# Kernel tuning notes

Hardware: AMD Instinct MI355X
Metric: run time of the kernel (lower is better)

Reference implementation:

```python
import jax, jax.numpy as jnp
import numpy as np

N_NODES = 100000


def sage_conv(x, src, dst, W_l, W_r, b):
    """PyG SAGEConv with mean aggregation: lin_l(mean_{j in N(i)} x_j) + lin_r(x_i) + b."""
    n = x.shape[0]
    msg = jax.ops.segment_sum(x[src], dst, num_segments=n)          # [N, C] sum of neighbor feats
    deg = jax.ops.segment_sum(jnp.ones_like(src, dtype=x.dtype), dst, num_segments=n)  # [N]
    agg = msg / jnp.maximum(deg, 1.0)[:, None]                      # mean aggregate
    return agg @ W_l + x @ W_r + b


def setup_inputs() -> dict:
    key = jax.random.key(0)
    ks = jax.random.split(key, 10)
    in_ch, hid, out_ch = 128, 128, 1
    E = 640000
    scale_in = 1.0 / np.sqrt(in_ch)
    scale_h = 1.0 / np.sqrt(hid)
    return {
        "x": jax.random.normal(ks[0], (N_NODES, in_ch), dtype=jnp.float32),
        "edge_index": jax.random.randint(ks[1], (2, E), 0, N_NODES, dtype=jnp.int64),
        "W1l": jax.random.normal(ks[2], (in_ch, hid), dtype=jnp.float32) * scale_in,
        "W1r": jax.random.normal(ks[3], (in_ch, hid), dtype=jnp.float32) * scale_in,
        "b1": jnp.zeros((hid,), dtype=jnp.float32),
        "W2l": jax.random.normal(ks[4], (hid, hid), dtype=jnp.float32) * scale_h,
        "W2r": jax.random.normal(ks[5], (hid, hid), dtype=jnp.float32) * scale_h,
        "b2": jnp.zeros((hid,), dtype=jnp.float32),
        "Wfc": jax.random.normal(ks[6], (hid, out_ch), dtype=jnp.float32) * scale_h,
        "bfc": jnp.zeros((out_ch,), dtype=jnp.float32),
    }


def reference(x, edge_index, W1l, W1r, b1, W2l, W2r, b2, Wfc, bfc):
    src, dst = edge_index[0], edge_index[1]
    h = sage_conv(x, src, dst, W1l, W1r, b1)
    h = jax.nn.relu(h)
    # dropout p=0.2 is identity in eval mode (training=False)
    h = sage_conv(h, src, dst, W2l, W2r, b2)
    h = jax.nn.relu(h)
    return jax.nn.sigmoid(h @ Wfc + bfc)
```

## Files before the change

### kernel.cpp

```cpp
#include <hip/hip_runtime.h>
#include <cstdint>

#define NN 100000
#define CH 128
#define NT_BLK 32
#define SCAN_B 256

typedef __bf16 bf16x8 __attribute__((ext_vector_type(8)));
typedef __bf16 bf16x4 __attribute__((ext_vector_type(4)));
typedef float  f32x4  __attribute__((ext_vector_type(4)));

__device__ __forceinline__ float b2f(unsigned short u) {
    union { unsigned int i; float f; } v; v.i = ((unsigned int)u) << 16; return v.f;
}

__global__ __launch_bounds__(256) void k_init(
    const float* __restrict__ x, unsigned short* __restrict__ xb,
    const float* __restrict__ W1l, const float* __restrict__ W1r,
    const float* __restrict__ W2l, const float* __restrict__ W2r,
    __bf16* __restrict__ wB, int* __restrict__ cnt)
{
    const int gtid = blockIdx.x * 256 + threadIdx.x;
    const int gsz = gridDim.x * 256;
    for (int i = gtid; i < NN; i += gsz) cnt[i] = 0;
    for (int i = gtid; i < NN * CH / 8; i += gsz) {
        const float4 a = *reinterpret_cast<const float4*>(x + (size_t)i * 8);
        const float4 c = *reinterpret_cast<const float4*>(x + (size_t)i * 8 + 4);
        bf16x8 o;
        o[0] = (__bf16)a.x; o[1] = (__bf16)a.y; o[2] = (__bf16)a.z; o[3] = (__bf16)a.w;
        o[4] = (__bf16)c.x; o[5] = (__bf16)c.y; o[6] = (__bf16)c.z; o[7] = (__bf16)c.w;
        *reinterpret_cast<bf16x8*>(xb + (size_t)i * 8) = o;
    }
    if (gtid < 8192) {
        const int l    = gtid >> 12;
        const int rem  = gtid & 4095;
        const int kt   = rem >> 9;
        const int nt   = (rem >> 6) & 7;
        const int lane = rem & 63;
        const float* Wl = l ? W2l : W1l;
        const float* Wr = l ? W2r : W1r;
        const int nn = nt * 16 + (lane & 15);
        const int k0 = kt * 32 + (lane >> 4) * 8;
        bf16x8 v;
#pragma unroll
        for (int i = 0; i < 8; ++i) {
            const int k = k0 + i;
            const float f = (k < CH) ? Wl[k * CH + nn] : Wr[(k - CH) * CH + nn];
            v[i] = (__bf16)f;
        }
        *reinterpret_cast<bf16x8*>(wB + (size_t)gtid * 8) = v;
    }
}

__global__ void k_count(const int* __restrict__ dst, int* __restrict__ cnt,
                        int* __restrict__ slot, int E) {
    const int e = blockIdx.x * blockDim.x + threadIdx.x;
    if (e < E) slot[e] = atomicAdd(&cnt[dst[e]], 1);
}

__global__ void k_scan(const int* __restrict__ cnt, int* __restrict__ rowptr,
                       int* __restrict__ bsum, int n) {
    __shared__ int tmp[SCAN_B];
    const int t = threadIdx.x;
    const int i = blockIdx.x * SCAN_B + t;
    const int v = (i < n) ? cnt[i] : 0;
    tmp[t] = v;
    __syncthreads();
    for (int off = 1; off < SCAN_B; off <<= 1) {
        const int tv = (t >= off) ? tmp[t - off] : 0;
        __syncthreads();
        tmp[t] += tv;
        __syncthreads();
    }
    if (i < n) rowptr[i] = tmp[t] - v;
    if (t == SCAN_B - 1) bsum[blockIdx.x] = tmp[SCAN_B - 1];
}

__global__ void k_add(int* __restrict__ rowptr, const int* __restrict__ bsum, int n, int E) {
    __shared__ int sd[SCAN_B];
    const int t = threadIdx.x;
    int s = 0;
    for (int j = t; j < (int)blockIdx.x; j += SCAN_B) s += bsum[j];
    sd[t] = s;
    __syncthreads();
    for (int off = SCAN_B / 2; off > 0; off >>= 1) {
        if (t < off) sd[t] += sd[t + off];
        __syncthreads();
    }
    const int base = sd[0];
    const int i = blockIdx.x * SCAN_B + t;
    if (i < n) rowptr[i] += base;
    if (i == 0) rowptr[n] = E;
}

__global__ void k_fill(const int* __restrict__ src, const int* __restrict__ dst,
                       const int* __restrict__ slot, const int* __restrict__ rowptr,
                       int* __restrict__ csr, int E) {
    const int e = blockIdx.x * blockDim.x + threadIdx.x;
    if (e < E) csr[rowptr[dst[e]] + slot[e]] = src[e];
}

template<bool FC>
__global__ __launch_bounds__(256) void k_layer(
    const unsigned short* __restrict__ feat,
    const int* __restrict__ rowptr, const int* __restrict__ csr,
    const bf16x8* __restrict__ wfrag,
    const float* __restrict__ bias,
    const float* __restrict__ Wfc, const float* __restrict__ bfc,
    void* __restrict__ outv)
{
    __shared__ unsigned short a_lds[NT_BLK * 256];
    __shared__ float red[4][16];
    char* lb = (char*)a_lds;
    const int tid = threadIdx.x;
    const int node0 = blockIdx.x * NT_BLK;

    const int g = tid >> 5;
    const int q = tid & 31;

#pragma unroll
    for (int it = 0; it < NT_BLK / 8; ++it) {
        const int r = it * 8 + g;
        const int node = node0 + r;
        const int swz = (r & 7) << 4;
        float4 s = make_float4(0.f, 0.f, 0.f, 0.f);
        bf16x4 k2 = {(__bf16)0.f, (__bf16)0.f, (__bf16)0.f, (__bf16)0.f};
        if (node < NN) {
            const int r0 = rowptr[node], r1 = rowptr[node + 1];
            const int last = r1 - 1;
            for (int rr = r0; rr < r1; rr += 8) {
                ushort4 uv[8];
                float mk[8];
#pragma unroll
                for (int u = 0; u < 8; ++u) {
                    const int p = rr + u;
                    const int idx = csr[p <= last ? p : last];
                    uv[u] = *reinterpret_cast<const ushort4*>(feat + (size_t)idx * CH + q * 4);
                    mk[u] = (p < r1) ? 1.f : 0.f;
                }
#pragma unroll
                for (int u = 0; u < 8; ++u) {
                    s.x += mk[u] * b2f(uv[u].x);
                    s.y += mk[u] * b2f(uv[u].y);
                    s.z += mk[u] * b2f(uv[u].z);
                    s.w += mk[u] * b2f(uv[u].w);
                }
            }
            const float invd = 1.0f / fmaxf((float)(r1 - r0), 1.0f);
            s.x *= invd; s.y *= invd; s.z *= invd; s.w *= invd;
            const ushort4 u = *reinterpret_cast<const ushort4*>(feat + (size_t)node * CH + q * 4);
            k2 = *reinterpret_cast<const bf16x4*>(&u);
        }
        bf16x4 a;
        a[0] = (__bf16)s.x; a[1] = (__bf16)s.y; a[2] = (__bf16)s.z; a[3] = (__bf16)s.w;
        *reinterpret_cast<bf16x4*>(lb + r * 512 + ((q * 8) ^ swz)) = a;
        *reinterpret_cast<bf16x4*>(lb + r * 512 + ((256 + q * 8) ^ swz)) = k2;
    }
    __syncthreads();

    const int lane = tid & 63;
    const int w = tid >> 6;
    const int rows16 = (w >> 1) * 16;
    const int ntbase = (w & 1) * 4;
    const int row = rows16 + (lane & 15);
    const int rswz = (row & 7) << 4;
    const int abase = row * 512;
    const int asub = (lane >> 4) * 16;

    f32x4 acc[4];
#pragma unroll
    for (int nt = 0; nt < 4; ++nt) { acc[nt][0] = 0.f; acc[nt][1] = 0.f; acc[nt][2] = 0.f; acc[nt][3] = 0.f; }

#pragma unroll
    for (int kt = 0; kt < 8; ++kt) {
        const bf16x8 a = *reinterpret_cast<const bf16x8*>(lb + abase + ((kt * 64 + asub) ^ rswz));
        const bf16x8* bp = wfrag + kt * 512 + ntbase * 64 + lane;
#pragma unroll
        for (int nt = 0; nt < 4; ++nt) {
            const bf16x8 b = bp[nt * 64];
            acc[nt] = __builtin_amdgcn_mfma_f32_16x16x32_bf16(a, b, acc[nt], 0, 0, 0);
        }
    }

    const int nbase = lane & 15;
    if (!FC) {
        __bf16* out = (__bf16*)outv;
#pragma unroll
        for (int nt = 0; nt < 4; ++nt) {
            const int ch = (ntbase + nt) * 16 + nbase;
            const float bv = bias[ch];
#pragma unroll
            for (int rr = 0; rr < 4; ++rr) {
                const int node = node0 + rows16 + (lane >> 4) * 4 + rr;
                if (node < NN)
                    out[(size_t)node * CH + ch] = (__bf16)fmaxf(acc[nt][rr] + bv, 0.0f);
            }
        }
    } else {
        float* out = (float*)outv;
        float p[4] = {0.f, 0.f, 0.f, 0.f};
#pragma unroll
        for (int nt = 0; nt < 4; ++nt) {
            const int ch = (ntbase + nt) * 16 + nbase;
            const float bv = bias[ch];
            const float wf = Wfc[ch];
#pragma unroll
            for (int rr = 0; rr < 4; ++rr)
                p[rr] += fmaxf(acc[nt][rr] + bv, 0.0f) * wf;
        }
#pragma unroll
        for (int m = 1; m < 16; m <<= 1) {
#pragma unroll
            for (int rr = 0; rr < 4; ++rr) p[rr] += __shfl_xor(p[rr], m);
        }
        if (nbase == 0) {
#pragma unroll
            for (int rr = 0; rr < 4; ++rr)
                red[w][(lane >> 4) * 4 + rr] = p[rr];
        }
        __syncthreads();
        if (tid < NT_BLK) {
            const int rloc = tid;
            const float z = (rloc < 16 ? red[0][rloc] + red[1][rloc]
                                       : red[2][rloc - 16] + red[3][rloc - 16]) + bfc[0];
            const int node = node0 + rloc;
            if (node < NN) out[node] = 1.0f / (1.0f + expf(-z));
        }
    }
}


extern "C" void kernel_launch(void* const* d_in, const int* in_sizes, int n_in,
                              void* d_out, int out_size, void* d_ws, size_t ws_size,
                              hipStream_t stream) {
    const float* x   = (const float*)d_in[0];
    const int*   ei  = (const int*)d_in[1];
    const float* W1l = (const float*)d_in[2];
    const float* W1r = (const float*)d_in[3];
    const float* b1  = (const float*)d_in[4];
    const float* W2l = (const float*)d_in[5];
    const float* W2r = (const float*)d_in[6];
    const float* b2  = (const float*)d_in[7];
    const float* Wfc = (const float*)d_in[8];
    const float* bfc = (const float*)d_in[9];

    const int E = in_sizes[1] / 2;
    const int* src = ei;
    const int* dst = ei + E;

    unsigned short* h1 = (unsigned short*)d_ws;
    unsigned short* xb = h1 + (size_t)NN * CH;
    __bf16* wB     = (__bf16*)(xb + (size_t)NN * CH);
    int*    cnt    = (int*)(wB + 65536);
    int*    rowptr = cnt + NN;
    int*    bsum   = rowptr + NN + 1;
    int*    slot   = bsum + 512;
    int*    csr    = slot + E;

    const int nb = (NN + SCAN_B - 1) / SCAN_B;
    const int eb = (E + 255) / 256;

    k_init<<<2048, 256, 0, stream>>>(x, xb, W1l, W1r, W2l, W2r, wB, cnt);
    k_count<<<eb, 256, 0, stream>>>(dst, cnt, slot, E);
    k_scan<<<nb, SCAN_B, 0, stream>>>(cnt, rowptr, bsum, NN);
    k_add<<<nb, SCAN_B, 0, stream>>>(rowptr, bsum, NN, E);
    k_fill<<<eb, 256, 0, stream>>>(src, dst, slot, rowptr, csr, E);

    const int blocks = (NN + NT_BLK - 1) / NT_BLK;
    k_layer<false><<<blocks, 256, 0, stream>>>(
        xb, rowptr, csr, (const bf16x8*)wB, b1, Wfc, bfc, h1);
    k_layer<true><<<blocks, 256, 0, stream>>>(
        h1, rowptr, csr, (const bf16x8*)(wB + 32768), b2, Wfc, bfc, d_out);
}
```

Baseline: 246.2 us.

## Merge preprocessing launches and use single-pass decoupled look-back scan

Zeroing of counters moves to a memset, and the edge counting, x-to-bf16 conversion and weight packing are merged into one block-partitioned kernel. The two-kernel scan plus add is replaced by a single-pass scan in which each block publishes its aggregate or inclusive prefix through flags and reads earlier blocks' values with a wavefront look-back. This removes kernel launches and the redundant per-block re-summing of block totals. In exchange, the scan now spin-waits on other blocks, which assumes earlier blocks are scheduled and make progress.

```diff
diff --git a/kernel.cpp b/kernel.cpp
--- a/kernel.cpp
+++ b/kernel.cpp
@@ -6,6 +6,10 @@
 #define NT_BLK 32
 #define SCAN_B 256
 
+#define AGG_F (1u << 30)
+#define PRE_F (2u << 30)
+#define VAL_M ((1u << 30) - 1)
+
 typedef __bf16 bf16x8 __attribute__((ext_vector_type(8)));
 typedef __bf16 bf16x4 __attribute__((ext_vector_type(4)));
 typedef float  f32x4  __attribute__((ext_vector_type(4)));
@@ -14,55 +18,61 @@
     union { unsigned int i; float f; } v; v.i = ((unsigned int)u) << 16; return v.f;
 }
 
-__global__ __launch_bounds__(256) void k_init(
+__global__ __launch_bounds__(256) void k_count_xw(
+    const int* __restrict__ dst, int* __restrict__ cnt, int* __restrict__ slot, int E,
     const float* __restrict__ x, unsigned short* __restrict__ xb,
     const float* __restrict__ W1l, const float* __restrict__ W1r,
     const float* __restrict__ W2l, const float* __restrict__ W2r,
-    __bf16* __restrict__ wB, int* __restrict__ cnt)
+    __bf16* __restrict__ wB, int eb, int xcb)
 {
-    const int gtid = blockIdx.x * 256 + threadIdx.x;
-    const int gsz = gridDim.x * 256;
-    for (int i = gtid; i < NN; i += gsz) cnt[i] = 0;
-    for (int i = gtid; i < NN * CH / 8; i += gsz) {
-        const float4 a = *reinterpret_cast<const float4*>(x + (size_t)i * 8);
-        const float4 c = *reinterpret_cast<const float4*>(x + (size_t)i * 8 + 4);
-        bf16x8 o;
-        o[0] = (__bf16)a.x; o[1] = (__bf16)a.y; o[2] = (__bf16)a.z; o[3] = (__bf16)a.w;
-        o[4] = (__bf16)c.x; o[5] = (__bf16)c.y; o[6] = (__bf16)c.z; o[7] = (__bf16)c.w;
-        *reinterpret_cast<bf16x8*>(xb + (size_t)i * 8) = o;
-    }
-    if (gtid < 8192) {
-        const int l    = gtid >> 12;
-        const int rem  = gtid & 4095;
-        const int kt   = rem >> 9;
-        const int nt   = (rem >> 6) & 7;
-        const int lane = rem & 63;
-        const float* Wl = l ? W2l : W1l;
-        const float* Wr = l ? W2r : W1r;
-        const int nn = nt * 16 + (lane & 15);
-        const int k0 = kt * 32 + (lane >> 4) * 8;
-        bf16x8 v;
-#pragma unroll
-        for (int i = 0; i < 8; ++i) {
-            const int k = k0 + i;
-            const float f = (k < CH) ? Wl[k * CH + nn] : Wr[(k - CH) * CH + nn];
-            v[i] = (__bf16)f;
-        }
-        *reinterpret_cast<bf16x8*>(wB + (size_t)gtid * 8) = v;
-    }
-}
-
-__global__ void k_count(const int* __restrict__ dst, int* __restrict__ cnt,
-                        int* __restrict__ slot, int E) {
-    const int e = blockIdx.x * blockDim.x + threadIdx.x;
-    if (e < E) slot[e] = atomicAdd(&cnt[dst[e]], 1);
-}
-
-__global__ void k_scan(const int* __restrict__ cnt, int* __restrict__ rowptr,
-                       int* __restrict__ bsum, int n) {
+    const int b = blockIdx.x;
+    const int t = threadIdx.x;
+    if (b < eb) {
+        const int e = b * 256 + t;
+        if (e < E) slot[e] = atomicAdd(&cnt[dst[e]], 1);
+        return;
+    }
+    if (b < eb + xcb) {
+        const size_t i = ((size_t)(b - eb) * 256 + t) * 8;
+        if (i < (size_t)NN * CH) {
+            const float4 a = *reinterpret_cast<const float4*>(x + i);
+            const float4 c = *reinterpret_cast<const float4*>(x + i + 4);
+            bf16x8 o;
+            o[0] = (__bf16)a.x; o[1] = (__bf16)a.y; o[2] = (__bf16)a.z; o[3] = (__bf16)a.w;
+            o[4] = (__bf16)c.x; o[5] = (__bf16)c.y; o[6] = (__bf16)c.z; o[7] = (__bf16)c.w;
+            *reinterpret_cast<bf16x8*>(xb + i) = o;
+        }
+        return;
+    }
+    const int gtid = (b - eb - xcb) * 256 + t;
+    const int l    = gtid >> 12;
+    const int rem  = gtid & 4095;
+    const int kt   = rem >> 9;
+    const int nt   = (rem >> 6) & 7;
+    const int lane = rem & 63;
+    const float* Wl = l ? W2l : W1l;
+    const float* Wr = l ? W2r : W1r;
+    const int nn = nt * 16 + (lane & 15);
+    const int k0 = kt * 32 + (lane >> 4) * 8;
+    bf16x8 v;
+#pragma unroll
+    for (int i = 0; i < 8; ++i) {
+        const int k = k0 + i;
+        const float f = (k < CH) ? Wl[k * CH + nn] : Wr[(k - CH) * CH + nn];
+        v[i] = (__bf16)f;
+    }
+    *reinterpret_cast<bf16x8*>(wB + (size_t)gtid * 8) = v;
+}
+
+__global__ __launch_bounds__(SCAN_B) void k_scan_lb(
+    const int* __restrict__ cnt, int* __restrict__ rowptr,
+    unsigned* __restrict__ flagval, int n, int E)
+{
     __shared__ int tmp[SCAN_B];
+    __shared__ int sbase;
     const int t = threadIdx.x;
-    const int i = blockIdx.x * SCAN_B + t;
+    const int c = blockIdx.x;
+    const int i = c * SCAN_B + t;
     const int v = (i < n) ? cnt[i] : 0;
     tmp[t] = v;
     __syncthreads();
@@ -72,24 +82,55 @@
         tmp[t] += tv;
         __syncthreads();
     }
-    if (i < n) rowptr[i] = tmp[t] - v;
-    if (t == SCAN_B - 1) bsum[blockIdx.x] = tmp[SCAN_B - 1];
-}
-
-__global__ void k_add(int* __restrict__ rowptr, const int* __restrict__ bsum, int n, int E) {
-    __shared__ int sd[SCAN_B];
-    const int t = threadIdx.x;
-    int s = 0;
-    for (int j = t; j < (int)blockIdx.x; j += SCAN_B) s += bsum[j];
-    sd[t] = s;
+    const int total = tmp[SCAN_B - 1];
+
+    if (c == 0) {
+        if (t == 0) {
+            sbase = 0;
+            __hip_atomic_store(&flagval[0], PRE_F | (unsigned)total,
+                               __ATOMIC_RELEASE, __HIP_MEMORY_SCOPE_AGENT);
+        }
+    } else {
+        if (t == 0)
+            __hip_atomic_store(&flagval[c], AGG_F | (unsigned)total,
+                               __ATOMIC_RELEASE, __HIP_MEMORY_SCOPE_AGENT);
+        if (t < 64) {
+            int base = 0;
+            int j = c - 1;
+            while (true) {
+                const int idx = j - t;
+                unsigned fv = 0;
+                if (idx >= 0) {
+                    do {
+                        fv = __hip_atomic_load(&flagval[idx], __ATOMIC_ACQUIRE,
+                                               __HIP_MEMORY_SCOPE_AGENT);
+                    } while ((fv >> 30) == 0);
+                }
+                const unsigned long long pmask = __ballot(idx >= 0 && (fv >> 30) == 2);
+                if (pmask) {
+                    const int firstPre = __ffsll(pmask) - 1;
+                    int contrib = (t <= firstPre && idx >= 0) ? (int)(fv & VAL_M) : 0;
+#pragma unroll
+                    for (int m = 1; m < 64; m <<= 1) contrib += __shfl_xor(contrib, m);
+                    base += contrib;
+                    break;
+                }
+                int contrib = (idx >= 0) ? (int)(fv & VAL_M) : 0;
+#pragma unroll
+                for (int m = 1; m < 64; m <<= 1) contrib += __shfl_xor(contrib, m);
+                base += contrib;
+                j -= 64;
+            }
+            if (t == 0) {
+                __hip_atomic_store(&flagval[c], PRE_F | (unsigned)(base + total),
+                                   __ATOMIC_RELEASE, __HIP_MEMORY_SCOPE_AGENT);
+                sbase = base;
+            }
+        }
+    }
     __syncthreads();
-    for (int off = SCAN_B / 2; off > 0; off >>= 1) {
-        if (t < off) sd[t] += sd[t + off];
-        __syncthreads();
-    }
-    const int base = sd[0];
-    const int i = blockIdx.x * SCAN_B + t;
-    if (i < n) rowptr[i] += base;
+    const int base = sbase;
+    if (i < n) rowptr[i] = tmp[t] - v + base;
     if (i == 0) rowptr[n] = E;
 }
 
@@ -250,20 +291,21 @@
 
     unsigned short* h1 = (unsigned short*)d_ws;
     unsigned short* xb = h1 + (size_t)NN * CH;
-    __bf16* wB     = (__bf16*)(xb + (size_t)NN * CH);
-    int*    cnt    = (int*)(wB + 65536);
-    int*    rowptr = cnt + NN;
-    int*    bsum   = rowptr + NN + 1;
-    int*    slot   = bsum + 512;
-    int*    csr    = slot + E;
-
-    const int nb = (NN + SCAN_B - 1) / SCAN_B;
-    const int eb = (E + 255) / 256;
-
-    k_init<<<2048, 256, 0, stream>>>(x, xb, W1l, W1r, W2l, W2r, wB, cnt);
-    k_count<<<eb, 256, 0, stream>>>(dst, cnt, slot, E);
-    k_scan<<<nb, SCAN_B, 0, stream>>>(cnt, rowptr, bsum, NN);
-    k_add<<<nb, SCAN_B, 0, stream>>>(rowptr, bsum, NN, E);
+    __bf16*   wB      = (__bf16*)(xb + (size_t)NN * CH);
+    int*      cnt     = (int*)(wB + 65536);
+    unsigned* flagval = (unsigned*)(cnt + NN);
+    int*      rowptr  = (int*)(flagval + 512);
+    int*      slot    = rowptr + NN + 1;
+    int*      csr     = slot + E;
+
+    const int nb  = (NN + SCAN_B - 1) / SCAN_B;
+    const int eb  = (E + 255) / 256;
+    const int xcb = (NN * CH) / 2048;
+
+    hipMemsetAsync(cnt, 0, (size_t)(NN + 512) * sizeof(int), stream);
+    k_count_xw<<<eb + xcb + 32, 256, 0, stream>>>(dst, cnt, slot, E, x, xb,
+                                                  W1l, W1r, W2l, W2r, wB, eb, xcb);
+    k_scan_lb<<<nb, SCAN_B, 0, stream>>>(cnt, rowptr, flagval, NN, E);
     k_fill<<<eb, 256, 0, stream>>>(src, dst, slot, rowptr, csr, E);
 
     const int blocks = (NN + NT_BLK - 1) / NT_BLK;
```

After: 257.4 us. 4.5% more time.
